# Optimization experiments

Hardware: AMD Instinct MI355X
Metric: run time of the kernel (lower is better)

Reference implementation:

```python
import jax, jax.numpy as jnp
import numpy as np

NUM_HEADS = 16
ROPE_THETA = 1000.0


def _rope(x, cos, sin):
    # x: [B, H, T, d_k]; cos/sin: [T, d_k//2]
    xp = x.reshape(x.shape[:-1] + (x.shape[-1] // 2, 2))
    xe, xo = xp[..., 0], xp[..., 1]
    c = cos[None, None, :, :]
    s = sin[None, None, :, :]
    re = xe * c - xo * s
    ro = xe * s + xo * c
    return jnp.stack((re, ro), axis=-1).reshape(x.shape)


def setup_inputs() -> dict:
    key = jax.random.key(0)
    ks = jax.random.split(key, 5)
    B, T, D = 2, 2048, 1024
    std = 2.0 / (D + D)
    return {
        "x": jax.random.normal(ks[0], (B, T, D), dtype=jnp.float32),
        "wq": jax.random.normal(ks[1], (D, D), dtype=jnp.float32) * std,
        "wk": jax.random.normal(ks[2], (D, D), dtype=jnp.float32) * std,
        "wv": jax.random.normal(ks[3], (D, D), dtype=jnp.float32) * std,
        "wo": jax.random.normal(ks[4], (D, D), dtype=jnp.float32) * std,
    }


def reference(x, wq, wk, wv, wo):
    B, T, D = x.shape
    H = NUM_HEADS
    dk = D // H

    def proj(w):
        # Linear stores weight as [out, in]: '... in, out in -> ... out'
        y = jnp.einsum('btd,ed->bte', x, w)
        return y.reshape(B, T, H, dk).transpose(0, 2, 1, 3)  # [B,H,T,dk]

    q = proj(wq)
    k = proj(wk)
    v = proj(wv)

    # RoPE tables
    pos = jnp.arange(T, dtype=jnp.float32)[:, None]
    kidx = jnp.arange(dk // 2, dtype=jnp.float32)
    inv_freq = ROPE_THETA ** (-2.0 * kidx / dk)
    ang = pos * inv_freq[None, :]
    cos, sin = jnp.cos(ang), jnp.sin(ang)

    q = _rope(q, cos, sin)
    k = _rope(k, cos, sin)

    scores = jnp.einsum('bhnd,bhmd->bhnm', q, k) / jnp.sqrt(jnp.asarray(dk, x.dtype))
    causal = jnp.tril(jnp.ones((T, T), dtype=bool))
    scores = jnp.where(causal[None, None], scores, -jnp.inf)
    attn = jax.nn.softmax(scores, axis=-1)
    head = jnp.einsum('bhnm,bhmd->bhnd', attn, v)  # [B,H,T,dk]

    concat = head.transpose(0, 2, 1, 3).reshape(B, T, D)
    return jnp.einsum('btd,ed->bte', concat, wo)
```

## Files before the change

### kernel.cpp

```cpp
#include <hip/hip_runtime.h>
#include <hip/hip_bf16.h>

typedef __hip_bfloat16 bf16;
typedef __attribute__((ext_vector_type(8))) short bf16x8;
typedef __attribute__((ext_vector_type(4))) float f32x4;

#define T_SEQ 2048
#define NHEADS 16
#define DK 64
#define DMODEL 1024

__device__ inline void load_lds16(const void* g, void* l) {
    __builtin_amdgcn_global_load_lds((const __attribute__((address_space(1))) void*)g,
                                     (__attribute__((address_space(3))) void*)l, 16, 0, 0);
}

__global__ void cvt_all(const float* __restrict__ x,  const float* __restrict__ wq,
                        const float* __restrict__ wk, const float* __restrict__ wv,
                        const float* __restrict__ wo, bf16* __restrict__ xb,
                        bf16* __restrict__ wqkvb, bf16* __restrict__ wob) {
    int i = blockIdx.x * blockDim.x + threadIdx.x;
    const float* src; bf16* dst; int off;
    if (i < (1 << 20)) { src = x; dst = xb; off = i; }
    else {
        int j = i - (1 << 20);
        int seg = j >> 18; off = j & ((1 << 18) - 1);
        src = (seg == 0) ? wq : (seg == 1) ? wk : (seg == 2) ? wv : wo;
        dst = (seg < 3) ? (wqkvb + ((size_t)seg << 20)) : wob;
    }
    float4 f = ((const float4*)src)[off];
    ushort4 o;
    o.x = __bfloat16_as_ushort(__float2bfloat16(f.x));
    o.y = __bfloat16_as_ushort(__float2bfloat16(f.y));
    o.z = __bfloat16_as_ushort(__float2bfloat16(f.z));
    o.w = __bfloat16_as_ushort(__float2bfloat16(f.w));
    ((ushort4*)dst)[off] = o;
}

__global__ __launch_bounds__(256) void gemm_qkv_rope(const bf16* __restrict__ A,
                                                     const bf16* __restrict__ B,
                                                     bf16* __restrict__ qb,
                                                     bf16* __restrict__ kb,
                                                     bf16* __restrict__ vt) {
    const int K = 1024, N = 3072;
    __shared__ bf16 As[128 * 32];
    __shared__ bf16 Bs[128 * 32];
    const int tid  = threadIdx.x;
    const int lane = tid & 63;
    const int wave = tid >> 6;
    const int l16  = lane & 15;
    const int quad = lane >> 4;
    const int wy = wave >> 1, wx = wave & 1;
    const int brow = blockIdx.y * 128;
    const int bcol = blockIdx.x * 128;

    f32x4 acc[4][4] = {};

    for (int k0 = 0; k0 < K; k0 += 32) {
#pragma unroll
        for (int i = 0; i < 2; ++i) {
            int j   = tid + 256 * i;
            int row = j >> 2;
            int cc  = j & 3;
            load_lds16(A + (size_t)(brow + row) * K + k0 + cc * 8, (char*)As + j * 16);
            load_lds16(B + (size_t)(bcol + row) * K + k0 + cc * 8, (char*)Bs + j * 16);
        }
        __syncthreads();
        bf16x8 af[4], bq[4];
#pragma unroll
        for (int i = 0; i < 4; ++i)
            af[i] = *(const bf16x8*)(As + (wy * 64 + i * 16 + l16) * 32 + quad * 8);
#pragma unroll
        for (int j = 0; j < 4; ++j)
            bq[j] = *(const bf16x8*)(Bs + (wx * 64 + j * 16 + l16) * 32 + quad * 8);
#pragma unroll
        for (int i = 0; i < 4; ++i)
#pragma unroll
            for (int j = 0; j < 4; ++j)
                acc[i][j] = __builtin_amdgcn_mfma_f32_16x16x32_bf16(af[i], bq[j], acc[i][j], 0, 0, 0);
        __syncthreads();
    }
    const int seg = bcol >> 10;
    const int hh  = ((bcol & 1023) >> 6) + wx;
    if (seg < 2) {
        bf16* dst = seg ? kb : qb;
#pragma unroll
        for (int j = 0; j < 4; ++j) {
            const int d = j * 16 + l16;
            const float inv = exp2f(-0.31143075889f * (float)(d >> 1));
#pragma unroll
            for (int i = 0; i < 4; ++i)
#pragma unroll
                for (int r = 0; r < 4; ++r) {
                    int row = brow + wy * 64 + i * 16 + quad * 4 + r;
                    int t = row & (T_SEQ - 1), bi = row >> 11;
                    float s, c;
                    __sincosf((float)t * inv, &s, &c);
                    float v = acc[i][j][r];
                    float p = __shfl_xor(v, 1);
                    float res = (l16 & 1) ? fmaf(p, s, v * c) : fmaf(-p, s, v * c);
                    dst[((size_t)(bi * NHEADS + hh) * T_SEQ + t) * DK + d] = __float2bfloat16(res);
                }
        }
    } else {
#pragma unroll
        for (int j = 0; j < 4; ++j) {
            const int d = j * 16 + l16;
#pragma unroll
            for (int i = 0; i < 4; ++i)
#pragma unroll
                for (int r = 0; r < 4; ++r) {
                    int row = brow + wy * 64 + i * 16 + quad * 4 + r;
                    int t = row & (T_SEQ - 1), bi = row >> 11;
                    vt[((size_t)(bi * NHEADS + hh) * DK + d) * T_SEQ + t] =
                        __float2bfloat16(acc[i][j][r]);
                }
        }
    }
}

__global__ __launch_bounds__(256) void gemm_bt(const bf16* __restrict__ A,
                                               const bf16* __restrict__ B,
                                               float* __restrict__ C,
                                               int M, int N, int K) {
    __shared__ bf16 As[128 * 32];
    __shared__ bf16 Bs[128 * 32];
    const int tid  = threadIdx.x;
    const int lane = tid & 63;
    const int wave = tid >> 6;
    const int l16  = lane & 15;
    const int quad = lane >> 4;
    const int wy = wave >> 1, wx = wave & 1;
    const int brow = blockIdx.y * 128;
    const int bcol = blockIdx.x * 128;

    f32x4 acc[4][4] = {};

    for (int k0 = 0; k0 < K; k0 += 32) {
#pragma unroll
        for (int i = 0; i < 2; ++i) {
            int j   = tid + 256 * i;
            int row = j >> 2;
            int cc  = j & 3;
            load_lds16(A + (size_t)(brow + row) * K + k0 + cc * 8, (char*)As + j * 16);
            load_lds16(B + (size_t)(bcol + row) * K + k0 + cc * 8, (char*)Bs + j * 16);
        }
        __syncthreads();
        bf16x8 af[4], bq[4];
#pragma unroll
        for (int i = 0; i < 4; ++i)
            af[i] = *(const bf16x8*)(As + (wy * 64 + i * 16 + l16) * 32 + quad * 8);
#pragma unroll
        for (int j = 0; j < 4; ++j)
            bq[j] = *(const bf16x8*)(Bs + (wx * 64 + j * 16 + l16) * 32 + quad * 8);
#pragma unroll
        for (int i = 0; i < 4; ++i)
#pragma unroll
            for (int j = 0; j < 4; ++j)
                acc[i][j] = __builtin_amdgcn_mfma_f32_16x16x32_bf16(af[i], bq[j], acc[i][j], 0, 0, 0);
        __syncthreads();
    }
#pragma unroll
    for (int i = 0; i < 4; ++i)
#pragma unroll
        for (int j = 0; j < 4; ++j)
#pragma unroll
            for (int r = 0; r < 4; ++r) {
                int row = brow + wy * 64 + i * 16 + quad * 4 + r;
                int col = bcol + wx * 64 + j * 16 + l16;
                C[(size_t)row * N + col] = acc[i][j][r];
            }
}

#define PSTRIDE 72
__global__ __launch_bounds__(256) void attn_kernel(const bf16* __restrict__ qb,
                                                   const bf16* __restrict__ kb,
                                                   const bf16* __restrict__ vt,
                                                   float* __restrict__ Oacc,
                                                   float* __restrict__ Lacc,
                                                   bf16* __restrict__ conc) {
    __shared__ bf16 Ks[2][64 * 64];
    __shared__ bf16 Vs[2][64 * 64];
    __shared__ bf16 Pl[4][16 * PSTRIDE];
    const int bh = blockIdx.y;
    const int b = bh >> 4, h = bh & 15;
    int x = 47 - (int)blockIdx.x;
    int tile, it0, it1;
    bool partial;
    if (x < 16) { tile = x; it0 = 0; it1 = tile; partial = false; }
    else {
        int idx = x - 16;
        tile = 16 + (idx >> 1);
        int mid = (tile + 1) >> 1;
        if (idx & 1) { it0 = mid; it1 = tile; } else { it0 = 0; it1 = mid - 1; }
        partial = true;
    }

    const int tid = threadIdx.x;
    const int lane = tid & 63, wave = tid >> 6;
    const int l16 = lane & 15, quad = lane >> 4;
    const int qrow = tile * 64 + wave * 16;

    const bf16* Qp = qb + (size_t)bh * T_SEQ * DK;
    const bf16* Kp = kb + (size_t)bh * T_SEQ * DK;
    const bf16* Vp = vt + (size_t)bh * DK * T_SEQ;
    bf16* Pw = &Pl[wave][0];

    bf16x8 qf[2];
#pragma unroll
    for (int s = 0; s < 2; ++s)
        qf[s] = *(const bf16x8*)(Qp + (size_t)(qrow + l16) * DK + s * 32 + quad * 8);

    auto stage = [&](int bb, int k0) {
        int j = tid;
#pragma unroll
        for (int i = 0; i < 2; ++i, j += 256) {
            int row = j >> 3, cbl = (j & 7) ^ ((j >> 3) & 7);
            load_lds16(Kp + (size_t)(k0 + row) * DK + cbl * 8, (char*)Ks[bb] + j * 16);
        }
        j = tid;
#pragma unroll
        for (int i = 0; i < 2; ++i, j += 256) {
            int row = j >> 3, cbl = (j & 7) ^ ((j >> 3) & 7);
            load_lds16(Vp + (size_t)row * T_SEQ + k0 + cbl * 8, (char*)Vs[bb] + j * 16);
        }
    };

    f32x4 o[4] = {};
    float l_i = 0.0f;
    const float ksc = 0.18033688011112042f;
    const int sw0 = (quad ^ (l16 & 7)) * 8;
    const int sw1 = ((4 + quad) ^ (l16 & 7)) * 8;

    int cur = 0;
    stage(0, it0 * 64);
    for (int it = it0; it <= it1; ++it) {
        __syncthreads();
        if (it < it1) stage(cur ^ 1, (it + 1) * 64);

        f32x4 sacc[4] = {};
#pragma unroll
        for (int nt = 0; nt < 4; ++nt) {
            bf16x8 kf0 = *(const bf16x8*)(Ks[cur] + (nt * 16 + l16) * 64 + sw0);
            bf16x8 kf1 = *(const bf16x8*)(Ks[cur] + (nt * 16 + l16) * 64 + sw1);
            sacc[nt] = __builtin_amdgcn_mfma_f32_16x16x32_bf16(kf0, qf[0], sacc[nt], 0, 0, 0);
            sacc[nt] = __builtin_amdgcn_mfma_f32_16x16x32_bf16(kf1, qf[1], sacc[nt], 0, 0, 0);
        }
        const int k0 = it * 64;
        const bool masked = (it == tile);
#pragma unroll
        for (int nt = 0; nt < 4; ++nt) {
            union { bf16 hv[4]; uint2 u; } pk;
#pragma unroll
            for (int r = 0; r < 4; ++r) {
                float v = sacc[nt][r] * ksc;
                if (masked && (k0 + nt * 16 + quad * 4 + r > qrow + l16)) v = -30.0f;
                float p = exp2f(v);
                l_i += p;
                pk.hv[r] = __float2bfloat16(p);
            }
            *(uint2*)(Pw + l16 * PSTRIDE + nt * 16 + quad * 4) = pk.u;
        }
#pragma unroll
        for (int ks = 0; ks < 2; ++ks) {
            bf16x8 pf = *(const bf16x8*)(Pw + l16 * PSTRIDE + ks * 32 + quad * 8);
            const int sw = ks ? sw1 : sw0;
#pragma unroll
            for (int j = 0; j < 4; ++j) {
                bf16x8 vf = *(const bf16x8*)(Vs[cur] + (j * 16 + l16) * 64 + sw);
                o[j] = __builtin_amdgcn_mfma_f32_16x16x32_bf16(pf, vf, o[j], 0, 0, 0);
            }
        }
        cur ^= 1;
    }
    float lt = l_i;
    lt += __shfl_xor(lt, 16);
    lt += __shfl_xor(lt, 32);
    if (!partial) {
#pragma unroll
        for (int r = 0; r < 4; ++r) {
            float lr = __shfl(lt, quad * 4 + r);
            float inv_l = 1.0f / lr;
            int t = qrow + quad * 4 + r;
#pragma unroll
            for (int j = 0; j < 4; ++j)
                conc[((size_t)b * T_SEQ + t) * DMODEL + h * DK + j * 16 + l16] =
                    __float2bfloat16(o[j][r] * inv_l);
        }
    } else {
        if (quad == 0)
            atomicAdd(&Lacc[(size_t)bh * 1024 + qrow + l16 - 1024], lt);
#pragma unroll
        for (int r = 0; r < 4; ++r) {
            int q = qrow + quad * 4 + r;
            float* Ob = Oacc + ((size_t)bh * 1024 + q - 1024) * DK;
#pragma unroll
            for (int j = 0; j < 4; ++j)
                atomicAdd(&Ob[j * 16 + l16], o[j][r]);
        }
    }
}

__global__ void attn_finalize(const float* __restrict__ Oacc, const float* __restrict__ Lacc,
                              bf16* __restrict__ conc) {
    int i4 = blockIdx.x * blockDim.x + threadIdx.x;
    if (i4 >= (1 << 19)) return;
    int bhq = i4 >> 4;
    int d4  = i4 & 15;
    int bh = bhq >> 10, q1 = bhq & 1023;
    int b = bh >> 4, h = bh & 15;
    int q = 1024 + q1;
    float inv = 1.0f / Lacc[bhq];
    float4 o4 = ((const float4*)Oacc)[i4];
    ushort4 u;
    u.x = __bfloat16_as_ushort(__float2bfloat16(o4.x * inv));
    u.y = __bfloat16_as_ushort(__float2bfloat16(o4.y * inv));
    u.z = __bfloat16_as_ushort(__float2bfloat16(o4.z * inv));
    u.w = __bfloat16_as_ushort(__float2bfloat16(o4.w * inv));
    *(ushort4*)&conc[((size_t)(b * T_SEQ + q)) * DMODEL + h * DK + d4 * 4] = u;
}

extern "C" void kernel_launch(void* const* d_in, const int* in_sizes, int n_in,
                              void* d_out, int out_size, void* d_ws, size_t ws_size,
                              hipStream_t stream) {
    const float* x  = (const float*)d_in[0];
    const float* wq = (const float*)d_in[1];
    const float* wk = (const float*)d_in[2];
    const float* wv = (const float*)d_in[3];
    const float* wo = (const float*)d_in[4];
    float* out = (float*)d_out;

    char* ws = (char*)d_ws;
    bf16* xb    = (bf16*)(ws);
    bf16* wqkvb = (bf16*)(ws + (8ull << 20));
    bf16* wob   = (bf16*)(ws + (14ull << 20));
    bf16* qb    = (bf16*)(ws + (40ull << 20));
    bf16* kb    = (bf16*)(ws + (48ull << 20));
    bf16* vt    = (bf16*)(ws + (56ull << 20));
    bf16* conc  = (bf16*)(ws + (16ull << 20));
    float* Oacc = (float*)(ws + (24ull << 20));
    float* Lacc = (float*)(ws + (32ull << 20));

    cvt_all<<<8192, 256, 0, stream>>>(x, wq, wk, wv, wo, xb, wqkvb, wob);
    gemm_qkv_rope<<<dim3(24, 32), 256, 0, stream>>>(xb, wqkvb, qb, kb, vt);

    hipMemsetAsync(Oacc, 0, (8ull << 20) + 32 * 1024 * sizeof(float), stream);
    attn_kernel<<<dim3(48, 32), 256, 0, stream>>>(qb, kb, vt, Oacc, Lacc, conc);
    attn_finalize<<<2048, 256, 0, stream>>>(Oacc, Lacc, conc);

    gemm_bt<<<dim3(8, 32), 256, 0, stream>>>(conc, wob, out, 4096, 1024, 1024);
}
```

Before: 220.2 us.

## Process 128 query rows per attention block with constant-table split schedule

Each attention block now handles two 64-row query groups (128 rows) against shared K/V tiles, so every staged K/V tile is used twice and global/LDS traffic per query is halved. Work is assigned through a constant schedule table that encodes tile and split mode, and the grid shrinks from 48 to 24 blocks per head. The softmax scale is folded into Q during the QKV/RoPE epilogue, which removes a multiply per score. In exchange each block holds more registers (two output accumulators), there are fewer blocks, and load balance now depends on the hand-made schedule.

```diff
diff --git a/kernel.cpp b/kernel.cpp
--- a/kernel.cpp
+++ b/kernel.cpp
@@ -84,6 +84,7 @@
     const int hh  = ((bcol & 1023) >> 6) + wx;
     if (seg < 2) {
         bf16* dst = seg ? kb : qb;
+        const float osc = seg ? 1.0f : 0.18033688011112042f;
 #pragma unroll
         for (int j = 0; j < 4; ++j) {
             const int d = j * 16 + l16;
@@ -99,7 +100,8 @@
                     float v = acc[i][j][r];
                     float p = __shfl_xor(v, 1);
                     float res = (l16 & 1) ? fmaf(p, s, v * c) : fmaf(-p, s, v * c);
-                    dst[((size_t)(bi * NHEADS + hh) * T_SEQ + t) * DK + d] = __float2bfloat16(res);
+                    dst[((size_t)(bi * NHEADS + hh) * T_SEQ + t) * DK + d] =
+                        __float2bfloat16(res * osc);
                 }
         }
     } else {
@@ -173,6 +175,11 @@
 }
 
 #define PSTRIDE 72
+__constant__ unsigned char c_sched[24] = {
+    28, 61, 57, 58, 24, 53, 49, 20,
+    62, 54, 50, 41, 42, 16, 45, 46,
+     0,  4,  8, 12, 33, 37, 34, 38};
+
 __global__ __launch_bounds__(256) void attn_kernel(const bf16* __restrict__ qb,
                                                    const bf16* __restrict__ kb,
                                                    const bf16* __restrict__ vt,
@@ -181,35 +188,35 @@
                                                    bf16* __restrict__ conc) {
     __shared__ bf16 Ks[2][64 * 64];
     __shared__ bf16 Vs[2][64 * 64];
-    __shared__ bf16 Pl[4][16 * PSTRIDE];
+    __shared__ bf16 Pl[4][2][16 * PSTRIDE];
     const int bh = blockIdx.y;
     const int b = bh >> 4, h = bh & 15;
-    int x = 47 - (int)blockIdx.x;
-    int tile, it0, it1;
-    bool partial;
-    if (x < 16) { tile = x; it0 = 0; it1 = tile; partial = false; }
-    else {
-        int idx = x - 16;
-        tile = 16 + (idx >> 1);
-        int mid = (tile + 1) >> 1;
-        if (idx & 1) { it0 = mid; it1 = tile; } else { it0 = 0; it1 = mid - 1; }
-        partial = true;
-    }
+
+    const int e    = c_sched[blockIdx.x];
+    const int tile = e >> 2, mode = e & 3;
+    const int it0  = (mode == 2) ? tile + 1 : 0;
+    const int it1  = (mode == 1) ? tile : 2 * tile + 1;
+    const bool partial = (mode != 0);
+    const int qbase = tile << 7;
 
     const int tid = threadIdx.x;
     const int lane = tid & 63, wave = tid >> 6;
     const int l16 = lane & 15, quad = lane >> 4;
-    const int qrow = tile * 64 + wave * 16;
+    const int qr0 = qbase + wave * 16;
+    const int qr1 = qr0 + 64;
 
     const bf16* Qp = qb + (size_t)bh * T_SEQ * DK;
     const bf16* Kp = kb + (size_t)bh * T_SEQ * DK;
     const bf16* Vp = vt + (size_t)bh * DK * T_SEQ;
-    bf16* Pw = &Pl[wave][0];
-
-    bf16x8 qf[2];
-#pragma unroll
-    for (int s = 0; s < 2; ++s)
-        qf[s] = *(const bf16x8*)(Qp + (size_t)(qrow + l16) * DK + s * 32 + quad * 8);
+    bf16* Pw0 = &Pl[wave][0][0];
+    bf16* Pw1 = &Pl[wave][1][0];
+
+    bf16x8 qf[2][2];
+#pragma unroll
+    for (int s = 0; s < 2; ++s) {
+        qf[0][s] = *(const bf16x8*)(Qp + (size_t)(qr0 + l16) * DK + s * 32 + quad * 8);
+        qf[1][s] = *(const bf16x8*)(Qp + (size_t)(qr1 + l16) * DK + s * 32 + quad * 8);
+    }
 
     auto stage = [&](int bb, int k0) {
         int j = tid;
@@ -226,9 +233,8 @@
         }
     };
 
-    f32x4 o[4] = {};
-    float l_i = 0.0f;
-    const float ksc = 0.18033688011112042f;
+    f32x4 o0[4] = {}, o1[4] = {};
+    float l0 = 0.0f, l1 = 0.0f;
     const int sw0 = (quad ^ (l16 & 7)) * 8;
     const int sw1 = ((4 + quad) ^ (l16 & 7)) * 8;
 
@@ -238,65 +244,103 @@
         __syncthreads();
         if (it < it1) stage(cur ^ 1, (it + 1) * 64);
 
-        f32x4 sacc[4] = {};
+        const int k0 = it * 64;
+        const bool skip0 = (k0 > qr0 + 15);
+        const bool diag0 = (k0 + 63 > qr0) && !skip0;
+        const bool diag1 = (k0 + 63 > qr1);
+
+        f32x4 s0[4] = {}, s1[4] = {};
 #pragma unroll
         for (int nt = 0; nt < 4; ++nt) {
             bf16x8 kf0 = *(const bf16x8*)(Ks[cur] + (nt * 16 + l16) * 64 + sw0);
             bf16x8 kf1 = *(const bf16x8*)(Ks[cur] + (nt * 16 + l16) * 64 + sw1);
-            sacc[nt] = __builtin_amdgcn_mfma_f32_16x16x32_bf16(kf0, qf[0], sacc[nt], 0, 0, 0);
-            sacc[nt] = __builtin_amdgcn_mfma_f32_16x16x32_bf16(kf1, qf[1], sacc[nt], 0, 0, 0);
-        }
-        const int k0 = it * 64;
-        const bool masked = (it == tile);
+            if (!skip0) {
+                s0[nt] = __builtin_amdgcn_mfma_f32_16x16x32_bf16(kf0, qf[0][0], s0[nt], 0, 0, 0);
+                s0[nt] = __builtin_amdgcn_mfma_f32_16x16x32_bf16(kf1, qf[0][1], s0[nt], 0, 0, 0);
+            }
+            s1[nt] = __builtin_amdgcn_mfma_f32_16x16x32_bf16(kf0, qf[1][0], s1[nt], 0, 0, 0);
+            s1[nt] = __builtin_amdgcn_mfma_f32_16x16x32_bf16(kf1, qf[1][1], s1[nt], 0, 0, 0);
+        }
+        if (!skip0) {
+#pragma unroll
+            for (int nt = 0; nt < 4; ++nt) {
+                union { bf16 hv[4]; uint2 u; } pk;
+#pragma unroll
+                for (int r = 0; r < 4; ++r) {
+                    float v = s0[nt][r];
+                    if (diag0 && (k0 + nt * 16 + quad * 4 + r > qr0 + l16)) v = -30.0f;
+                    float p = exp2f(v);
+                    l0 += p;
+                    pk.hv[r] = __float2bfloat16(p);
+                }
+                *(uint2*)(Pw0 + l16 * PSTRIDE + nt * 16 + quad * 4) = pk.u;
+            }
+        }
 #pragma unroll
         for (int nt = 0; nt < 4; ++nt) {
             union { bf16 hv[4]; uint2 u; } pk;
 #pragma unroll
             for (int r = 0; r < 4; ++r) {
-                float v = sacc[nt][r] * ksc;
-                if (masked && (k0 + nt * 16 + quad * 4 + r > qrow + l16)) v = -30.0f;
+                float v = s1[nt][r];
+                if (diag1 && (k0 + nt * 16 + quad * 4 + r > qr1 + l16)) v = -30.0f;
                 float p = exp2f(v);
-                l_i += p;
+                l1 += p;
                 pk.hv[r] = __float2bfloat16(p);
             }
-            *(uint2*)(Pw + l16 * PSTRIDE + nt * 16 + quad * 4) = pk.u;
+            *(uint2*)(Pw1 + l16 * PSTRIDE + nt * 16 + quad * 4) = pk.u;
         }
 #pragma unroll
         for (int ks = 0; ks < 2; ++ks) {
-            bf16x8 pf = *(const bf16x8*)(Pw + l16 * PSTRIDE + ks * 32 + quad * 8);
             const int sw = ks ? sw1 : sw0;
-#pragma unroll
-            for (int j = 0; j < 4; ++j) {
-                bf16x8 vf = *(const bf16x8*)(Vs[cur] + (j * 16 + l16) * 64 + sw);
-                o[j] = __builtin_amdgcn_mfma_f32_16x16x32_bf16(pf, vf, o[j], 0, 0, 0);
-            }
+            bf16x8 vf[4];
+#pragma unroll
+            for (int j = 0; j < 4; ++j)
+                vf[j] = *(const bf16x8*)(Vs[cur] + (j * 16 + l16) * 64 + sw);
+            if (!skip0) {
+                bf16x8 pf0 = *(const bf16x8*)(Pw0 + l16 * PSTRIDE + ks * 32 + quad * 8);
+#pragma unroll
+                for (int j = 0; j < 4; ++j)
+                    o0[j] = __builtin_amdgcn_mfma_f32_16x16x32_bf16(pf0, vf[j], o0[j], 0, 0, 0);
+            }
+            bf16x8 pf1 = *(const bf16x8*)(Pw1 + l16 * PSTRIDE + ks * 32 + quad * 8);
+#pragma unroll
+            for (int j = 0; j < 4; ++j)
+                o1[j] = __builtin_amdgcn_mfma_f32_16x16x32_bf16(pf1, vf[j], o1[j], 0, 0, 0);
         }
         cur ^= 1;
     }
-    float lt = l_i;
-    lt += __shfl_xor(lt, 16);
-    lt += __shfl_xor(lt, 32);
-    if (!partial) {
-#pragma unroll
-        for (int r = 0; r < 4; ++r) {
-            float lr = __shfl(lt, quad * 4 + r);
-            float inv_l = 1.0f / lr;
-            int t = qrow + quad * 4 + r;
-#pragma unroll
-            for (int j = 0; j < 4; ++j)
-                conc[((size_t)b * T_SEQ + t) * DMODEL + h * DK + j * 16 + l16] =
-                    __float2bfloat16(o[j][r] * inv_l);
-        }
-    } else {
-        if (quad == 0)
-            atomicAdd(&Lacc[(size_t)bh * 1024 + qrow + l16 - 1024], lt);
-#pragma unroll
-        for (int r = 0; r < 4; ++r) {
-            int q = qrow + quad * 4 + r;
-            float* Ob = Oacc + ((size_t)bh * 1024 + q - 1024) * DK;
-#pragma unroll
-            for (int j = 0; j < 4; ++j)
-                atomicAdd(&Ob[j * 16 + l16], o[j][r]);
+#pragma unroll
+    for (int g = 0; g < 2; ++g) {
+        float lt = g ? l1 : l0;
+        lt += __shfl_xor(lt, 16);
+        lt += __shfl_xor(lt, 32);
+        const int qr = g ? qr1 : qr0;
+        if (!partial) {
+#pragma unroll
+            for (int r = 0; r < 4; ++r) {
+                float lr = __shfl(lt, quad * 4 + r);
+                float inv_l = 1.0f / lr;
+                int t = qr + quad * 4 + r;
+#pragma unroll
+                for (int j = 0; j < 4; ++j) {
+                    float ov = g ? o1[j][r] : o0[j][r];
+                    conc[((size_t)b * T_SEQ + t) * DMODEL + h * DK + j * 16 + l16] =
+                        __float2bfloat16(ov * inv_l);
+                }
+            }
+        } else {
+            if (quad == 0)
+                atomicAdd(&Lacc[(size_t)bh * 1024 + qr + l16 - 1024], lt);
+#pragma unroll
+            for (int r = 0; r < 4; ++r) {
+                int q = qr + quad * 4 + r;
+                float* Ob = Oacc + ((size_t)bh * 1024 + q - 1024) * DK;
+#pragma unroll
+                for (int j = 0; j < 4; ++j) {
+                    float ov = g ? o1[j][r] : o0[j][r];
+                    atomicAdd(&Ob[j * 16 + l16], ov);
+                }
+            }
         }
     }
 }
@@ -345,7 +389,7 @@
     gemm_qkv_rope<<<dim3(24, 32), 256, 0, stream>>>(xb, wqkvb, qb, kb, vt);
 
     hipMemsetAsync(Oacc, 0, (8ull << 20) + 32 * 1024 * sizeof(float), stream);
-    attn_kernel<<<dim3(48, 32), 256, 0, stream>>>(qb, kb, vt, Oacc, Lacc, conc);
+    attn_kernel<<<dim3(24, 32), 256, 0, stream>>>(qb, kb, vt, Oacc, Lacc, conc);
     attn_finalize<<<2048, 256, 0, stream>>>(Oacc, Lacc, conc);
 
     gemm_bt<<<dim3(8, 32), 256, 0, stream>>>(conc, wob, out, 4096, 1024, 1024);
```

New measurement: 210.2 us. 4.6% less time.
